# Kernel optimization log

Measured on AMD Instinct MI355X. Metric: run time of the kernel, lower is better.

Reference implementation:

```python
import jax, jax.numpy as jnp
import numpy as np

BS, NQ, NC, NT = 16, 900, 91, 1600
COST_CLASS, COST_BBOX, COST_GIOU = 1.0, 5.0, 2.0


def box_cxcywh_to_xyxy(b):
    cx, cy, w, h = b[..., 0], b[..., 1], b[..., 2], b[..., 3]
    return jnp.stack([cx - 0.5 * w, cy - 0.5 * h, cx + 0.5 * w, cy + 0.5 * h], axis=-1)


def generalized_box_iou(boxes1, boxes2):
    # boxes1: [N,4] xyxy, boxes2: [M,4] xyxy -> [N,M]
    area1 = (boxes1[:, 2] - boxes1[:, 0]) * (boxes1[:, 3] - boxes1[:, 1])  # [N]
    area2 = (boxes2[:, 2] - boxes2[:, 0]) * (boxes2[:, 3] - boxes2[:, 1])  # [M]
    lt = jnp.maximum(boxes1[:, None, :2], boxes2[None, :, :2])  # [N,M,2]
    rb = jnp.minimum(boxes1[:, None, 2:], boxes2[None, :, 2:])  # [N,M,2]
    wh = jnp.clip(rb - lt, 0.0)
    inter = wh[..., 0] * wh[..., 1]  # [N,M]
    union = area1[:, None] + area2[None, :] - inter
    iou = inter / union
    # smallest enclosing box
    lt_c = jnp.minimum(boxes1[:, None, :2], boxes2[None, :, :2])
    rb_c = jnp.maximum(boxes1[:, None, 2:], boxes2[None, :, 2:])
    wh_c = jnp.clip(rb_c - lt_c, 0.0)
    area_c = wh_c[..., 0] * wh_c[..., 1]
    return iou - (area_c - union) / area_c


def setup_inputs() -> dict:
    key = jax.random.key(0)
    k1, k2, k3, k4 = jax.random.split(key, 4)
    pred_logits = jax.random.normal(k1, (BS, NQ, NC), dtype=jnp.float32)
    # cxcywh in (0,1): guarantee positive w,h and sane boxes
    pred_boxes = jax.random.uniform(k2, (BS, NQ, 4), dtype=jnp.float32, minval=0.05, maxval=0.95)
    tgt_bbox = jax.random.uniform(k3, (NT, 4), dtype=jnp.float32, minval=0.05, maxval=0.95)
    tgt_ids = jax.random.randint(k4, (NT,), 0, NC, dtype=jnp.int32)
    return {"pred_logits": pred_logits, "pred_boxes": pred_boxes,
            "tgt_bbox": tgt_bbox, "tgt_ids": tgt_ids}


def reference(pred_logits, pred_boxes, tgt_bbox, tgt_ids):
    bs, num_queries = pred_logits.shape[:2]
    out_prob = jax.nn.softmax(pred_logits.reshape(-1, pred_logits.shape[-1]), axis=-1)  # [bs*nq, NC]
    out_bbox = pred_boxes.reshape(-1, 4)  # [bs*nq, 4]
    cost_class = -out_prob[:, tgt_ids]  # [bs*nq, NT]
    # L1 cdist
    cost_bbox = jnp.sum(jnp.abs(out_bbox[:, None, :] - tgt_bbox[None, :, :]), axis=-1)
    cost_giou = -generalized_box_iou(box_cxcywh_to_xyxy(out_bbox), box_cxcywh_to_xyxy(tgt_bbox))
    C = COST_BBOX * cost_bbox + COST_CLASS * cost_class + COST_GIOU * cost_giou
    return C.reshape(bs, num_queries, -1)
```

## Files before the change

kernel.cpp:

```cpp
#include <hip/hip_runtime.h>
#include <math.h>

#define BS_ 16
#define NQ_ 900
#define NC_ 91
#define NT_ 1600
#define NROWS_ (BS_ * NQ_)

__global__ __launch_bounds__(256) void matcher_cost_kernel(
    const float* __restrict__ logits,
    const float* __restrict__ pboxes,
    const float* __restrict__ tboxes,
    const int*   __restrict__ tids,
    float* __restrict__ out)
{
    const int row  = blockIdx.x;
    const int tid  = threadIdx.x;
    const int lane = tid & 63;
    const int wave = tid >> 6;

    __shared__ float sprob[NC_];
    __shared__ float sred[4];

    const float* lrow = logits + (size_t)row * NC_;
    float v = (tid < NC_) ? lrow[tid] : -INFINITY;

    float m = v;
    #pragma unroll
    for (int off = 32; off >= 1; off >>= 1)
        m = fmaxf(m, __shfl_xor(m, off, 64));
    if (lane == 0) sred[wave] = m;
    __syncthreads();
    m = fmaxf(fmaxf(sred[0], sred[1]), fmaxf(sred[2], sred[3]));

    float e = (tid < NC_) ? __expf(v - m) : 0.0f;
    float s = e;
    #pragma unroll
    for (int off = 32; off >= 1; off >>= 1)
        s += __shfl_xor(s, off, 64);
    __syncthreads();
    if (lane == 0) sred[wave] = s;
    __syncthreads();
    s = sred[0] + sred[1] + sred[2] + sred[3];
    const float inv_s = 1.0f / s;
    if (tid < NC_) sprob[tid] = e * inv_s;
    __syncthreads();

    const float4 qb = *reinterpret_cast<const float4*>(pboxes + (size_t)row * 4);
    const float qx0 = qb.x - 0.5f * qb.z, qy0 = qb.y - 0.5f * qb.w;
    const float qx1 = qb.x + 0.5f * qb.z, qy1 = qb.y + 0.5f * qb.w;
    const float qarea = qb.z * qb.w;

    float* orow = out + (size_t)row * NT_;

    for (int j = tid; j < NT_; j += 256) {
        const float4 tb = *reinterpret_cast<const float4*>(tboxes + (size_t)j * 4);
        const int id = tids[j];

        const float cb = fabsf(qb.x - tb.x) + fabsf(qb.y - tb.y)
                       + fabsf(qb.z - tb.z) + fabsf(qb.w - tb.w);

        const float tx0 = tb.x - 0.5f * tb.z, ty0 = tb.y - 0.5f * tb.w;
        const float tx1 = tb.x + 0.5f * tb.z, ty1 = tb.y + 0.5f * tb.w;
        const float tarea = tb.z * tb.w;

        float iw = fminf(qx1, tx1) - fmaxf(qx0, tx0);
        float ih = fminf(qy1, ty1) - fmaxf(qy0, ty0);
        iw = fmaxf(iw, 0.0f);
        ih = fmaxf(ih, 0.0f);
        const float inter = iw * ih;
        const float uni   = qarea + tarea - inter;
        const float iou   = inter / uni;

        const float cw = fmaxf(qx1, tx1) - fminf(qx0, tx0);
        const float ch = fmaxf(qy1, ty1) - fminf(qy0, ty0);
        const float areac = fmaxf(cw, 0.0f) * fmaxf(ch, 0.0f);
        const float giou  = iou - (areac - uni) / areac;

        orow[j] = 5.0f * cb - sprob[id] - 2.0f * giou;
    }
}

extern "C" void kernel_launch(void* const* d_in, const int* in_sizes, int n_in,
                              void* d_out, int out_size, void* d_ws, size_t ws_size,
                              hipStream_t stream) {
    const float* logits = (const float*)d_in[0];
    const float* pboxes = (const float*)d_in[1];
    const float* tboxes = (const float*)d_in[2];
    const int*   tids   = (const int*)d_in[3];
    float* out = (float*)d_out;

    matcher_cost_kernel<<<NROWS_, 256, 0, stream>>>(logits, pboxes, tboxes, tids, out);
}
```

Baseline: 134.5 us.

## Process four query rows per block with per-wave softmax and reused target loads

Each block now handles four query rows. Each wave computes the softmax of one row using shuffles only, which removes the shared-memory reductions and the extra barriers. Target box and class-id loads are reused across the four rows, and the probabilities are stored interleaved so one float4 LDS read fetches all four. The divides become rcp approximations folded into FMAs, and the output uses nontemporal stores. These changes add precision risk from rcpf and drop the clamp on the enclosing box size.

Result: faster. 120.0 us (-10.8%).

```diff
diff --git a/kernel.cpp b/kernel.cpp
--- a/kernel.cpp
+++ b/kernel.cpp
@@ -6,89 +6,101 @@
 #define NC_ 91
 #define NT_ 1600
 #define NROWS_ (BS_ * NQ_)
+#define TILE_R 4
+#define NBLK (NROWS_ / TILE_R)
 
 __global__ __launch_bounds__(256) void matcher_cost_kernel(
     const float* __restrict__ logits,
     const float* __restrict__ pboxes,
-    const float* __restrict__ tboxes,
+    const float4* __restrict__ tboxes,
     const int*   __restrict__ tids,
     float* __restrict__ out)
 {
-    const int row  = blockIdx.x;
+    const int base = blockIdx.x * TILE_R;
     const int tid  = threadIdx.x;
     const int lane = tid & 63;
     const int wave = tid >> 6;
 
-    __shared__ float sprob[NC_];
-    __shared__ float sred[4];
+    __shared__ __align__(16) float sprob_t[NC_ * TILE_R];
 
-    const float* lrow = logits + (size_t)row * NC_;
-    float v = (tid < NC_) ? lrow[tid] : -INFINITY;
-
-    float m = v;
-    #pragma unroll
-    for (int off = 32; off >= 1; off >>= 1)
-        m = fmaxf(m, __shfl_xor(m, off, 64));
-    if (lane == 0) sred[wave] = m;
-    __syncthreads();
-    m = fmaxf(fmaxf(sred[0], sred[1]), fmaxf(sred[2], sred[3]));
-
-    float e = (tid < NC_) ? __expf(v - m) : 0.0f;
-    float s = e;
-    #pragma unroll
-    for (int off = 32; off >= 1; off >>= 1)
-        s += __shfl_xor(s, off, 64);
-    __syncthreads();
-    if (lane == 0) sred[wave] = s;
-    __syncthreads();
-    s = sred[0] + sred[1] + sred[2] + sred[3];
-    const float inv_s = 1.0f / s;
-    if (tid < NC_) sprob[tid] = e * inv_s;
+    {
+        const float* lrow = logits + (size_t)(base + wave) * NC_;
+        float v0 = lrow[lane];
+        float v1 = (lane < NC_ - 64) ? lrow[64 + lane] : -INFINITY;
+        float m = fmaxf(v0, v1);
+        #pragma unroll
+        for (int off = 32; off >= 1; off >>= 1)
+            m = fmaxf(m, __shfl_xor(m, off, 64));
+        float e0 = __expf(v0 - m);
+        float e1 = (lane < NC_ - 64) ? __expf(v1 - m) : 0.0f;
+        float s = e0 + e1;
+        #pragma unroll
+        for (int off = 32; off >= 1; off >>= 1)
+            s += __shfl_xor(s, off, 64);
+        const float inv_s = __builtin_amdgcn_rcpf(s);
+        sprob_t[lane * TILE_R + wave] = e0 * inv_s;
+        if (lane < NC_ - 64)
+            sprob_t[(64 + lane) * TILE_R + wave] = e1 * inv_s;
+    }
     __syncthreads();
 
-    const float4 qb = *reinterpret_cast<const float4*>(pboxes + (size_t)row * 4);
-    const float qx0 = qb.x - 0.5f * qb.z, qy0 = qb.y - 0.5f * qb.w;
-    const float qx1 = qb.x + 0.5f * qb.z, qy1 = qb.y + 0.5f * qb.w;
-    const float qarea = qb.z * qb.w;
-
-    float* orow = out + (size_t)row * NT_;
+    float qcx[TILE_R], qcy[TILE_R], qw[TILE_R], qh[TILE_R];
+    float qx0[TILE_R], qy0[TILE_R], qx1[TILE_R], qy1[TILE_R], qarea[TILE_R];
+    #pragma unroll
+    for (int r = 0; r < TILE_R; ++r) {
+        const float4 qb = *reinterpret_cast<const float4*>(pboxes + (size_t)(base + r) * 4);
+        qcx[r] = qb.x; qcy[r] = qb.y; qw[r] = qb.z; qh[r] = qb.w;
+        qx0[r] = fmaf(-0.5f, qb.z, qb.x);
+        qy0[r] = fmaf(-0.5f, qb.w, qb.y);
+        qx1[r] = fmaf( 0.5f, qb.z, qb.x);
+        qy1[r] = fmaf( 0.5f, qb.w, qb.y);
+        qarea[r] = qb.z * qb.w;
+    }
 
     for (int j = tid; j < NT_; j += 256) {
-        const float4 tb = *reinterpret_cast<const float4*>(tboxes + (size_t)j * 4);
+        const float4 tb = tboxes[j];
         const int id = tids[j];
 
-        const float cb = fabsf(qb.x - tb.x) + fabsf(qb.y - tb.y)
-                       + fabsf(qb.z - tb.z) + fabsf(qb.w - tb.w);
-
-        const float tx0 = tb.x - 0.5f * tb.z, ty0 = tb.y - 0.5f * tb.w;
-        const float tx1 = tb.x + 0.5f * tb.z, ty1 = tb.y + 0.5f * tb.w;
+        const float tx0 = fmaf(-0.5f, tb.z, tb.x);
+        const float ty0 = fmaf(-0.5f, tb.w, tb.y);
+        const float tx1 = fmaf( 0.5f, tb.z, tb.x);
+        const float ty1 = fmaf( 0.5f, tb.w, tb.y);
         const float tarea = tb.z * tb.w;
 
-        float iw = fminf(qx1, tx1) - fmaxf(qx0, tx0);
-        float ih = fminf(qy1, ty1) - fmaxf(qy0, ty0);
-        iw = fmaxf(iw, 0.0f);
-        ih = fmaxf(ih, 0.0f);
-        const float inter = iw * ih;
-        const float uni   = qarea + tarea - inter;
-        const float iou   = inter / uni;
+        const float4 p4 = *reinterpret_cast<const float4*>(&sprob_t[id * TILE_R]);
+        const float p[TILE_R] = {p4.x, p4.y, p4.z, p4.w};
 
-        const float cw = fmaxf(qx1, tx1) - fminf(qx0, tx0);
-        const float ch = fmaxf(qy1, ty1) - fminf(qy0, ty0);
-        const float areac = fmaxf(cw, 0.0f) * fmaxf(ch, 0.0f);
-        const float giou  = iou - (areac - uni) / areac;
+        #pragma unroll
+        for (int r = 0; r < TILE_R; ++r) {
+            const float cb = fabsf(qcx[r] - tb.x) + fabsf(qcy[r] - tb.y)
+                           + fabsf(qw[r]  - tb.z) + fabsf(qh[r]  - tb.w);
 
-        orow[j] = 5.0f * cb - sprob[id] - 2.0f * giou;
+            const float iw = fmaxf(fminf(qx1[r], tx1) - fmaxf(qx0[r], tx0), 0.0f);
+            const float ih = fmaxf(fminf(qy1[r], ty1) - fmaxf(qy0[r], ty0), 0.0f);
+            const float inter = iw * ih;
+            const float uni   = qarea[r] + tarea - inter;
+
+            const float cw = fmaxf(qx1[r], tx1) - fminf(qx0[r], tx0);
+            const float ch = fmaxf(qy1[r], ty1) - fminf(qy0[r], ty0);
+            const float areac = cw * ch;
+
+            float c = fmaf(5.0f, cb, 2.0f - p[r]);
+            c = fmaf(-2.0f * inter, __builtin_amdgcn_rcpf(uni),   c);
+            c = fmaf(-2.0f * uni,   __builtin_amdgcn_rcpf(areac), c);
+
+            __builtin_nontemporal_store(c, out + (size_t)(base + r) * NT_ + j);
+        }
     }
 }
 
 extern "C" void kernel_launch(void* const* d_in, const int* in_sizes, int n_in,
                               void* d_out, int out_size, void* d_ws, size_t ws_size,
                               hipStream_t stream) {
-    const float* logits = (const float*)d_in[0];
-    const float* pboxes = (const float*)d_in[1];
-    const float* tboxes = (const float*)d_in[2];
-    const int*   tids   = (const int*)d_in[3];
+    const float*  logits = (const float*)d_in[0];
+    const float*  pboxes = (const float*)d_in[1];
+    const float4* tboxes = (const float4*)d_in[2];
+    const int*    tids   = (const int*)d_in[3];
     float* out = (float*)d_out;
 
-    matcher_cost_kernel<<<NROWS_, 256, 0, stream>>>(logits, pboxes, tboxes, tids, out);
+    matcher_cost_kernel<<<NBLK, 256, 0, stream>>>(logits, pboxes, tboxes, tids, out);
 }
```
